# Kernel optimization log

Measured on AMD Instinct MI355X. Metric: run time of the kernel, lower is better.

Reference implementation:

```python
import jax, jax.numpy as jnp
import numpy as np

T, HID, H, KV, D = 2048, 2048, 16, 8, 128
EPS = 1e-6
THETA = 10000.0


def setup_inputs() -> dict:
    key = jax.random.key(0)
    ks = jax.random.split(key, 6)
    positions = jnp.arange(T, dtype=jnp.int64 if jax.config.jax_enable_x64 else jnp.int32)
    hidden_states = jax.random.normal(ks[0], (T, HID), dtype=jnp.float32)
    scale = 0.02
    Wq = jax.random.normal(ks[1], (HID, H * 2 * D), dtype=jnp.float32) * scale
    Wk = jax.random.normal(ks[2], (HID, KV * D), dtype=jnp.float32) * scale
    Wv = jax.random.normal(ks[3], (HID, KV * D), dtype=jnp.float32) * scale
    Wo = jax.random.normal(ks[4], (H * D, HID), dtype=jnp.float32) * scale
    q_norm_w = jnp.zeros((D,), dtype=jnp.float32)  # torch init: zeros, applied as (1+w)
    k_norm_w = jnp.zeros((D,), dtype=jnp.float32)
    return {"positions": positions, "hidden_states": hidden_states, "Wq": Wq,
            "Wk": Wk, "Wv": Wv, "Wo": Wo, "q_norm_w": q_norm_w, "k_norm_w": k_norm_w}


def _rms_norm(x, w):
    # fp32 RMSNorm with (1 + weight) scaling, per last dim
    xf = x.astype(jnp.float32)
    inv = jax.lax.rsqrt(jnp.mean(xf * xf, axis=-1, keepdims=True) + EPS)
    return (xf * inv * (1.0 + w.astype(jnp.float32))).astype(x.dtype)


def _rope(x, positions):
    # neox-style rotary over full head_dim; x: (T, heads, D)
    half = D // 2
    inv_freq = 1.0 / (THETA ** (jnp.arange(0, half, dtype=jnp.float32) / half))
    freqs = positions.astype(jnp.float32)[:, None] * inv_freq  # (T, half)
    cos = jnp.cos(freqs)[:, None, :]  # (T,1,half)
    sin = jnp.sin(freqs)[:, None, :]
    x1, x2 = x[..., :half], x[..., half:]
    return jnp.concatenate([x1 * cos - x2 * sin, x2 * cos + x1 * sin], axis=-1)


def reference(positions, hidden_states, Wq, Wk, Wv, Wo, q_norm_w, k_norm_w):
    scaling = D ** -0.5
    qg = (hidden_states @ Wq).reshape(T, H, 2 * D)
    q, gate = qg[..., :D], qg[..., D:]              # (T,H,D) each
    k = (hidden_states @ Wk).reshape(T, KV, D)
    v = (hidden_states @ Wv).reshape(T, KV, D)
    q = _rms_norm(q, q_norm_w)
    k = _rms_norm(k, k_norm_w)
    q = _rope(q, positions)
    k = _rope(k, positions)
    # GQA: repeat kv heads
    rep = H // KV
    k = jnp.repeat(k, rep, axis=1)                   # (T,H,D)
    v = jnp.repeat(v, rep, axis=1)
    scores = jnp.einsum('thd,shd->hts', q, k) * scaling  # (H,T,T)
    causal = positions[:, None] >= positions[None, :]     # (T,T)
    scores = jnp.where(causal[None], scores, jnp.finfo(scores.dtype).min)
    probs = jax.nn.softmax(scores, axis=-1)
    o = jnp.einsum('hts,shd->thd', probs, v).reshape(T, H * D)
    o = o * jax.nn.sigmoid(gate.reshape(T, H * D))
    return o @ Wo
```

## Files before the change

### kernel.cpp

```cpp
#include <hip/hip_runtime.h>
#include <stdint.h>
#include <math.h>

#define T_SEQ 2048
#define HID   2048
#define NH    16
#define NKV   8
#define DH    128

typedef __bf16 bf16x8 __attribute__((ext_vector_type(8)));
typedef float  f32x4  __attribute__((ext_vector_type(4)));

__device__ __forceinline__ ushort f2bf(float f) {
  uint32_t u = __float_as_uint(f);
  u += 0x7FFF + ((u >> 16) & 1);
  return (ushort)(u >> 16);
}
__device__ __forceinline__ ushort f2bf_rz(float f) {
  return (ushort)(__float_as_uint(f) >> 16);
}
__device__ __forceinline__ float bf2f(ushort u) {
  return __uint_as_float(((uint32_t)u) << 16);
}
__device__ __forceinline__ void gld16(const void* g, void* l) {
  __builtin_amdgcn_global_load_lds(
      (const __attribute__((address_space(1))) uint32_t*)g,
      (__attribute__((address_space(3))) uint32_t*)l, 16, 0, 0);
}

__global__ __launch_bounds__(256) void prep_kernel(
    const float* __restrict__ hs, const float* __restrict__ Wq,
    const float* __restrict__ Wk, const float* __restrict__ Wv,
    const float* __restrict__ Wo, ushort* __restrict__ hs16,
    ushort* __restrict__ Wqt, ushort* __restrict__ Wkt,
    ushort* __restrict__ Wvt, ushort* __restrict__ Wot) {
  int bid = blockIdx.x;
  if (bid < 4096) {
    int i = (bid * 256 + threadIdx.x) * 4;
    float4 v = *(const float4*)(hs + i);
    ushort4 o = {f2bf(v.x), f2bf(v.y), f2bf(v.z), f2bf(v.w)};
    *(ushort4*)(hs16 + i) = o;
    return;
  }
  bid -= 4096;
  const float* src; ushort* dst; int N, bi, bj;
  if (bid < 2048)      { src = Wq; dst = Wqt; N = 4096; bj = bid & 63; bi = bid >> 6; }
  else if (bid < 2560) { bid -= 2048; src = Wk; dst = Wkt; N = 1024; bj = bid & 15; bi = bid >> 4; }
  else if (bid < 3072) { bid -= 2560; src = Wv; dst = Wvt; N = 1024; bj = bid & 15; bi = bid >> 4; }
  else                 { bid -= 3072; src = Wo; dst = Wot; N = 2048; bj = bid & 31; bi = bid >> 5; }
  __shared__ float tile[64][65];
  const int r = threadIdx.x >> 2, cg = (threadIdx.x & 3) * 16;
  const float* sp = src + (size_t)(bi * 64 + r) * N + bj * 64 + cg;
#pragma unroll
  for (int p = 0; p < 4; ++p) {
    float4 v = *(const float4*)(sp + p * 4);
    tile[r][cg + p * 4 + 0] = v.x; tile[r][cg + p * 4 + 1] = v.y;
    tile[r][cg + p * 4 + 2] = v.z; tile[r][cg + p * 4 + 3] = v.w;
  }
  __syncthreads();
  ushort* dp = dst + (size_t)(bj * 64 + r) * HID + bi * 64 + cg;
#pragma unroll
  for (int p = 0; p < 2; ++p) {
    union { uint4 v; ushort u[8]; } o;
#pragma unroll
    for (int j = 0; j < 8; ++j) o.u[j] = f2bf(tile[cg + p * 8 + j][r]);
    *(uint4*)(dp + p * 8) = o.v;
  }
}

template <int MI>
__device__ __forceinline__ void gemm_loop(
    const ushort* __restrict__ A, const ushort* __restrict__ Bt,
    int K, int m0, int n0, ushort* As, ushort* Bs, f32x4 (*acc)[4]) {
  const int tid = threadIdx.x, lane = tid & 63, w = tid >> 6;
  const int quad = lane >> 4, l15 = lane & 15;
  const int wm = (w >> 1) * (MI * 16), wn = (w & 1) * 64;
  const int srow = tid >> 2, sch = tid & 3;
  for (int k0 = 0; k0 < K; k0 += 32) {
    __syncthreads();
#pragma unroll
    for (int p = 0; p < MI / 2; ++p) {
      int row = p * 64 + srow;
      int gch = sch ^ ((row >> 1) & 3);
      gld16(A + (size_t)(m0 + row) * K + k0 + gch * 8,
            As + (p * 256 + w * 64) * 8);
    }
#pragma unroll
    for (int p = 0; p < 2; ++p) {
      int row = p * 64 + srow;
      int gch = sch ^ ((row >> 1) & 3);
      gld16(Bt + (size_t)(n0 + row) * K + k0 + gch * 8,
            Bs + (p * 256 + w * 64) * 8);
    }
    __syncthreads();
    bf16x8 af[MI], bfr[4];
#pragma unroll
    for (int mi = 0; mi < MI; ++mi) {
      int row = wm + mi * 16 + l15;
      int pch = quad ^ ((row >> 1) & 3);
      af[mi] = *(const bf16x8*)(As + row * 32 + pch * 8);
    }
#pragma unroll
    for (int ni = 0; ni < 4; ++ni) {
      int row = wn + ni * 16 + l15;
      int pch = quad ^ ((row >> 1) & 3);
      bfr[ni] = *(const bf16x8*)(Bs + row * 32 + pch * 8);
    }
#pragma unroll
    for (int mi = 0; mi < MI; ++mi)
#pragma unroll
      for (int ni = 0; ni < 4; ++ni)
        acc[mi][ni] = __builtin_amdgcn_mfma_f32_16x16x32_bf16(
            af[mi], bfr[ni], acc[mi][ni], 0, 0, 0);
  }
}

__device__ __forceinline__ void bf16_store(f32x4 (*acc)[4],
                                           ushort* __restrict__ Cb, int Ncols,
                                           int m0, int n0) {
  const int lane = threadIdx.x & 63, w = threadIdx.x >> 6;
  const int quad = lane >> 4, l15 = lane & 15;
  const int wm = (w >> 1) * 64, wn = (w & 1) * 64;
#pragma unroll
  for (int mi = 0; mi < 4; ++mi)
#pragma unroll
    for (int ni = 0; ni < 4; ++ni)
#pragma unroll
      for (int r = 0; r < 4; ++r) {
        int row = m0 + wm + mi * 16 + quad * 4 + r;
        int col = n0 + wn + ni * 16 + l15;
        Cb[(size_t)row * Ncols + col] = f2bf(acc[mi][ni][r]);
      }
}

__global__ __launch_bounds__(256) void gemm_qkv(
    const ushort* __restrict__ hs16, const ushort* __restrict__ Wqt,
    const ushort* __restrict__ Wkt, const ushort* __restrict__ Wvt,
    ushort* __restrict__ qg16, ushort* __restrict__ kb16,
    ushort* __restrict__ v16t) {
  __shared__ ushort As[128 * 32];
  __shared__ ushort Bs[128 * 32];
  f32x4 acc[4][4];
#pragma unroll
  for (int i = 0; i < 4; ++i)
#pragma unroll
    for (int j = 0; j < 4; ++j) acc[i][j] = (f32x4){0.f, 0.f, 0.f, 0.f};
  const int b = blockIdx.x;
  if (b < 512) {
    int m0 = (b >> 5) * 128, n0 = (b & 31) * 128;
    gemm_loop<4>(hs16, Wqt, HID, m0, n0, As, Bs, acc);
    bf16_store(acc, qg16, 4096, m0, n0);
  } else if (b < 640) {
    int f = b - 512, m0 = (f >> 3) * 128, n0 = (f & 7) * 128;
    gemm_loop<4>(hs16, Wkt, HID, m0, n0, As, Bs, acc);
    bf16_store(acc, kb16, 1024, m0, n0);
  } else {
    int f = b - 640, m0 = (f >> 4) * 128, n0 = (f & 15) * 128;
    gemm_loop<4>(Wvt, hs16, HID, m0, n0, As, Bs, acc);
    bf16_store(acc, v16t, T_SEQ, m0, n0);
  }
}

__global__ __launch_bounds__(256) void gemm_out(
    const ushort* __restrict__ ob16, const ushort* __restrict__ Wot,
    float* __restrict__ out) {
  __shared__ ushort As[64 * 32];
  __shared__ ushort Bs[128 * 32];
  f32x4 acc[2][4];
#pragma unroll
  for (int i = 0; i < 2; ++i)
#pragma unroll
    for (int j = 0; j < 4; ++j) acc[i][j] = (f32x4){0.f, 0.f, 0.f, 0.f};
  const int b = blockIdx.x;
  const int m0 = (b >> 4) * 64, n0 = (b & 15) * 128;
  gemm_loop<2>(ob16, Wot, HID, m0, n0, As, Bs, acc);
  const int lane = threadIdx.x & 63, w = threadIdx.x >> 6;
  const int quad = lane >> 4, l15 = lane & 15;
  const int wm = (w >> 1) * 32, wn = (w & 1) * 64;
#pragma unroll
  for (int mi = 0; mi < 2; ++mi)
#pragma unroll
    for (int ni = 0; ni < 4; ++ni)
#pragma unroll
      for (int r = 0; r < 4; ++r) {
        int row = m0 + wm + mi * 16 + quad * 4 + r;
        int col = n0 + wn + ni * 16 + l15;
        out[(size_t)row * HID + col] = acc[mi][ni][r];
      }
}

__global__ __launch_bounds__(128) void norm_k(
    const ushort* __restrict__ kb16, const int* __restrict__ positions,
    const float* __restrict__ kw, ushort* __restrict__ k16) {
  const int t = blockIdx.x, kv = blockIdx.y, d = threadIdx.x;
  const ushort* x = kb16 + ((size_t)t * NKV + kv) * DH;
  ushort* out = k16 + ((size_t)t * NKV + kv) * DH;
  float v = bf2f(x[d]);
  float ss = v * v;
#pragma unroll
  for (int off = 32; off >= 1; off >>= 1) ss += __shfl_xor(ss, off, 64);
  __shared__ float red[2];
  if ((d & 63) == 0) red[d >> 6] = ss;
  __syncthreads();
  float mean = (red[0] + red[1]) * (1.0f / 128.0f);
  float xn = v * rsqrtf(mean + 1e-6f) * (1.0f + kw[d]);
  __shared__ float sh[128];
  sh[d] = xn;
  __syncthreads();
  if (d < 64) {
    float pos = (float)positions[t];
    float rev = pos * exp2f((float)d * -0.20762050593045233f) *
                0.15915494309189535f;
    float fr = rev - floorf(rev);
    float s = __builtin_amdgcn_sinf(fr);
    float c = __builtin_amdgcn_cosf(fr);
    float x1 = sh[d], x2 = sh[d + 64];
    out[d]      = f2bf(x1 * c - x2 * s);
    out[d + 64] = f2bf(x2 * c + x1 * s);
  }
}

__global__ __launch_bounds__(256) void attn_mfma(
    const ushort* __restrict__ qg16, const ushort* __restrict__ k16,
    const ushort* __restrict__ v16t, const int* __restrict__ positions,
    const float* __restrict__ qnw, const float* __restrict__ knw,
    ushort* __restrict__ Op0, ushort* __restrict__ Op1,
    ushort* __restrict__ Op2, float* __restrict__ lpart) {
  const int pb = blockIdx.x, h = blockIdx.y, s = blockIdx.z, kvh = h >> 1;
  const int tid = threadIdx.x, lane = tid & 63, w = tid >> 6;
  const int quad = lane >> 4, l15 = lane & 15;

  __shared__ ushort Ks[64 * 128];
  __shared__ ushort Vs[144 * 64];
  __shared__ ushort Ps[4][16][72];

  for (int i = tid; i < 16 * 64; i += 256) {
    int row = 128 + (i >> 6), col = i & 63;
    Vs[row * 64 + col] = (row == 128) ? (ushort)0x3F80 : (ushort)0;
  }

  __shared__ float s8[8];
  __shared__ float bshare;
  {
    float mq = 0.f, mk = 0.f;
    if (tid < 128) { mq = fabsf(1.f + qnw[tid]); mk = fabsf(1.f + knw[tid]); }
#pragma unroll
    for (int off = 32; off >= 1; off >>= 1) {
      mq = fmaxf(mq, __shfl_xor(mq, off, 64));
      mk = fmaxf(mk, __shfl_xor(mk, off, 64));
    }
    if (lane == 0) { s8[w * 2] = mq; s8[w * 2 + 1] = mk; }
    __syncthreads();
    if (tid == 0) {
      float MQ = fmaxf(s8[0], s8[2]), MK = fmaxf(s8[1], s8[3]);
      bshare = 16.3217f * MQ * MK * 1.02f + 0.1f;
    }
    __syncthreads();
  }
  const float B = bshare;
  const float CSC = 0.08838834764831845f * 1.44269504088896f;

  float wq[4][8];
#pragma unroll
  for (int ks = 0; ks < 4; ++ks)
#pragma unroll
    for (int j = 0; j < 8; ++j) wq[ks][j] = 1.f + qnw[ks * 32 + quad * 8 + j];

#pragma unroll 1
  for (int sel = 0; sel < 2; ++sel) {
    const int qt = sel ? (31 - pb) : pb;
    const int q0 = qt * 64;
    const int ntl = (qt >= s) ? ((qt - s) / 3 + 1) : 0;

    float qv[4][8];
    const ushort* qb = qg16 + ((size_t)(q0 + w * 16 + l15) * NH + h) * (2 * DH);
#pragma unroll
    for (int ks = 0; ks < 4; ++ks) {
      ushort4 u0 = *(const ushort4*)(qb + ks * 32 + quad * 8);
      ushort4 u1 = *(const ushort4*)(qb + ks * 32 + quad * 8 + 4);
      qv[ks][0] = bf2f(u0.x); qv[ks][1] = bf2f(u0.y);
      qv[ks][2] = bf2f(u0.z); qv[ks][3] = bf2f(u0.w);
      qv[ks][4] = bf2f(u1.x); qv[ks][5] = bf2f(u1.y);
      qv[ks][6] = bf2f(u1.z); qv[ks][7] = bf2f(u1.w);
    }
    float ss = 0.f;
#pragma unroll
    for (int ks = 0; ks < 4; ++ks)
#pragma unroll
      for (int j = 0; j < 8; ++j) ss += qv[ks][j] * qv[ks][j];
    ss += __shfl_xor(ss, 16, 64);
    ss += __shfl_xor(ss, 32, 64);
    const float inv = rsqrtf(ss * (1.f / 128.f) + 1e-6f);
    const float pos = (float)positions[q0 + w * 16 + l15];
    union { bf16x8 v; ushort u[8]; } qfu[4];
#pragma unroll
    for (int ks = 0; ks < 2; ++ks)
#pragma unroll
      for (int j = 0; j < 8; ++j) {
        int d = ks * 32 + quad * 8 + j;
        float rev = pos * exp2f((float)d * -0.20762050593045233f) *
                    0.15915494309189535f;
        float fr = rev - floorf(rev);
        float sn = __builtin_amdgcn_sinf(fr);
        float cs = __builtin_amdgcn_cosf(fr);
        float x1 = qv[ks][j] * inv * wq[ks][j];
        float x2 = qv[ks + 2][j] * inv * wq[ks + 2][j];
        qfu[ks].u[j]     = f2bf(x1 * cs - x2 * sn);
        qfu[ks + 2].u[j] = f2bf(x2 * cs + x1 * sn);
      }

    f32x4 oacc[9];
#pragma unroll
    for (int i = 0; i < 9; ++i) oacc[i] = (f32x4){0.f, 0.f, 0.f, 0.f};

#pragma unroll 1
    for (int it = 0; it < ntl; ++it) {
      const int kt = s + 3 * it;
      const int kt0 = kt * 64;
      __syncthreads();
#pragma unroll
      for (int p = 0; p < 4; ++p) {
        int row = p * 16 + (tid >> 4), ch = tid & 15;
        int gch = ch ^ (row & 15);
        gld16(k16 + ((size_t)(kt0 + row) * NKV + kvh) * DH + gch * 8,
              Ks + (p * 256 + w * 64) * 8);
      }
#pragma unroll
      for (int p = 0; p < 4; ++p) {
        int row = p * 32 + (tid >> 3), ch = tid & 7;
        int gch = ch ^ (row & 7);
        gld16(v16t + (size_t)(kvh * DH + row) * T_SEQ + kt0 + gch * 8,
              Vs + (p * 256 + w * 64) * 8);
      }
      __syncthreads();

      f32x4 sacc[4];
#pragma unroll
      for (int ni = 0; ni < 4; ++ni) sacc[ni] = (f32x4){0.f, 0.f, 0.f, 0.f};
#pragma unroll
      for (int ks = 0; ks < 4; ++ks)
#pragma unroll
        for (int ni = 0; ni < 4; ++ni) {
          int row = ni * 16 + l15;
          int pch = (ks * 4 + quad) ^ (row & 15);
          bf16x8 kf = *(const bf16x8*)(Ks + row * 128 + pch * 8);
          sacc[ni] = __builtin_amdgcn_mfma_f32_16x16x32_bf16(
              qfu[ks].v, kf, sacc[ni], 0, 0, 0);
        }

      const bool diag = (kt == qt);
#pragma unroll
      for (int ni = 0; ni < 4; ++ni) {
        int key = kt0 + ni * 16 + l15;
#pragma unroll
        for (int r = 0; r < 4; ++r) {
          float arg = fmaf(sacc[ni][r], CSC, -B);
          float pv;
          if (diag) {
            int q = q0 + w * 16 + quad * 4 + r;
            pv = (key <= q) ? exp2f(arg) : 0.f;
          } else {
            pv = exp2f(arg);
          }
          Ps[w][quad * 4 + r][ni * 16 + l15] = f2bf_rz(pv);
        }
      }

#pragma unroll
      for (int ks2 = 0; ks2 < 2; ++ks2) {
        bf16x8 pf = *(const bf16x8*)(&Ps[w][l15][ks2 * 32 + quad * 8]);
#pragma unroll
        for (int ni = 0; ni < 9; ++ni) {
          int row = ni * 16 + l15;
          int pch = (ks2 * 4 + quad) ^ (row & 7);
          bf16x8 vf = *(const bf16x8*)(Vs + row * 64 + pch * 8);
          oacc[ni] = __builtin_amdgcn_mfma_f32_16x16x32_bf16(
              pf, vf, oacc[ni], 0, 0, 0);
        }
      }
    }

    ushort* Op = (s == 0) ? Op0 : (s == 1) ? Op1 : Op2;
#pragma unroll
    for (int ni = 0; ni < 8; ++ni) {
      int d = ni * 16 + l15;
#pragma unroll
      for (int r = 0; r < 4; ++r) {
        int q = q0 + w * 16 + quad * 4 + r;
        Op[((size_t)h * T_SEQ + q) * DH + d] = f2bf(oacc[ni][r]);
      }
    }
    if (l15 == 0) {
#pragma unroll
      for (int r = 0; r < 4; ++r) {
        int q = q0 + w * 16 + quad * 4 + r;
        lpart[(size_t)s * (NH * T_SEQ) + h * T_SEQ + q] = oacc[8][r];
      }
    }
  }
}

__global__ __launch_bounds__(256) void combine_kernel(
    const ushort* __restrict__ Op0, const ushort* __restrict__ Op1,
    const ushort* __restrict__ Op2, const float* __restrict__ lpart,
    const ushort* __restrict__ qg16, ushort* __restrict__ ob16) {
  const int t = blockIdx.x, tid = threadIdx.x;
  const int h = tid >> 4, d0 = (tid & 15) * 8;
  const int NT = NH * T_SEQ;
  const float l = lpart[h * T_SEQ + t] + lpart[NT + h * T_SEQ + t] +
                  lpart[2 * NT + h * T_SEQ + t];
  const float inv = 1.0f / l;
  const size_t po = ((size_t)h * T_SEQ + t) * DH + d0;
  ushort4 a0 = *(const ushort4*)(Op0 + po);
  ushort4 a1 = *(const ushort4*)(Op0 + po + 4);
  ushort4 b0 = *(const ushort4*)(Op1 + po);
  ushort4 b1 = *(const ushort4*)(Op1 + po + 4);
  ushort4 c0 = *(const ushort4*)(Op2 + po);
  ushort4 c1 = *(const ushort4*)(Op2 + po + 4);
  const ushort* gp = qg16 + ((size_t)t * NH + h) * (2 * DH) + DH + d0;
  ushort4 g0 = *(const ushort4*)(gp);
  ushort4 g1 = *(const ushort4*)(gp + 4);
  float oa[8] = {bf2f(a0.x), bf2f(a0.y), bf2f(a0.z), bf2f(a0.w),
                 bf2f(a1.x), bf2f(a1.y), bf2f(a1.z), bf2f(a1.w)};
  float ob[8] = {bf2f(b0.x), bf2f(b0.y), bf2f(b0.z), bf2f(b0.w),
                 bf2f(b1.x), bf2f(b1.y), bf2f(b1.z), bf2f(b1.w)};
  float oc[8] = {bf2f(c0.x), bf2f(c0.y), bf2f(c0.z), bf2f(c0.w),
                 bf2f(c1.x), bf2f(c1.y), bf2f(c1.z), bf2f(c1.w)};
  float gg[8] = {bf2f(g0.x), bf2f(g0.y), bf2f(g0.z), bf2f(g0.w),
                 bf2f(g1.x), bf2f(g1.y), bf2f(g1.z), bf2f(g1.w)};
  ushort r[8];
#pragma unroll
  for (int i = 0; i < 8; ++i) {
    float o = (oa[i] + ob[i] + oc[i]) * inv;
    o = o / (1.0f + exp2f(-gg[i] * 1.44269504088896f));
    r[i] = f2bf(o);
  }
  ushort* op = ob16 + (size_t)t * (NH * DH) + h * DH + d0;
  *(ushort4*)(op)     = (ushort4){r[0], r[1], r[2], r[3]};
  *(ushort4*)(op + 4) = (ushort4){r[4], r[5], r[6], r[7]};
}

extern "C" void kernel_launch(void* const* d_in, const int* in_sizes, int n_in,
                              void* d_out, int out_size, void* d_ws, size_t ws_size,
                              hipStream_t stream) {
  const int*   positions = (const int*)d_in[0];
  const float* hs  = (const float*)d_in[1];
  const float* Wq  = (const float*)d_in[2];
  const float* Wk  = (const float*)d_in[3];
  const float* Wv  = (const float*)d_in[4];
  const float* Wo  = (const float*)d_in[5];
  const float* qnw = (const float*)d_in[6];
  const float* knw = (const float*)d_in[7];
  float* out = (float*)d_out;

  const size_t MB = 1 << 20;
  uint8_t* ws = (uint8_t*)d_ws;
  ushort* qg16 = (ushort*)(ws + 0);
  ushort* hs16 = (ushort*)(ws + 16 * MB);
  ushort* Op0  = (ushort*)(ws + 16 * MB);
  ushort* Wqt  = (ushort*)(ws + 24 * MB);
  ushort* Op1  = (ushort*)(ws + 24 * MB);
  ushort* Op2  = (ushort*)(ws + 32 * MB);
  ushort* kb16 = (ushort*)(ws + 40 * MB);
  float*  lpart= (float*)(ws + 40 * MB);
  ushort* Wkt  = (ushort*)(ws + 44 * MB);
  ushort* k16  = (ushort*)(ws + 44 * MB);
  ushort* Wvt  = (ushort*)(ws + 48 * MB);
  ushort* ob16 = (ushort*)(ws + 48 * MB);
  ushort* v16t = (ushort*)(ws + 52 * MB);
  ushort* Wot  = (ushort*)(ws + 56 * MB);

  prep_kernel<<<8192, 256, 0, stream>>>(hs, Wq, Wk, Wv, Wo,
                                        hs16, Wqt, Wkt, Wvt, Wot);
  gemm_qkv<<<768, 256, 0, stream>>>(hs16, Wqt, Wkt, Wvt, qg16, kb16, v16t);
  norm_k<<<dim3(T_SEQ, NKV), 128, 0, stream>>>(kb16, positions, knw, k16);
  attn_mfma<<<dim3(16, NH, 3), 256, 0, stream>>>(qg16, k16, v16t, positions,
                                                 qnw, knw, Op0, Op1, Op2, lpart);
  combine_kernel<<<T_SEQ, 256, 0, stream>>>(Op0, Op1, Op2, lpart, qg16, ob16);
  gemm_out<<<512, 256, 0, stream>>>(ob16, Wot, out);
}
```

Measured before the change: 289.5 us.

## Fuse Q/K RMSNorm and RoPE into the QKV GEMM epilogue

Moves the Q and K RMSNorm plus rotary embedding into the QKV GEMM epilogue. It remaps each warp's B-fragment columns so every thread holds both halves of each rotary pair, and reduces the row sum of squares through shared memory. This removes the separate norm_k launch and the per-tile Q norm/RoPE recomputation inside the attention kernel, which now loads pre-rotated bf16 Q directly. Gate is written to its own buffer, the workspace layout is reshuffled, and lpart temporarily lives in the output buffer. The cost is a heavier GEMM epilogue with scattered 2-byte stores and extra syncs.

```diff
diff --git a/kernel.cpp b/kernel.cpp
--- a/kernel.cpp
+++ b/kernel.cpp
@@ -68,13 +68,13 @@
   }
 }
 
-template <int MI>
+template <int MI, int REMAP>
 __device__ __forceinline__ void gemm_loop(
     const ushort* __restrict__ A, const ushort* __restrict__ Bt,
     int K, int m0, int n0, ushort* As, ushort* Bs, f32x4 (*acc)[4]) {
   const int tid = threadIdx.x, lane = tid & 63, w = tid >> 6;
   const int quad = lane >> 4, l15 = lane & 15;
-  const int wm = (w >> 1) * (MI * 16), wn = (w & 1) * 64;
+  const int wm = (w >> 1) * (MI * 16), wn = (w & 1) * 64, p32 = (w & 1) * 32;
   const int srow = tid >> 2, sch = tid & 3;
   for (int k0 = 0; k0 < K; k0 += 32) {
     __syncthreads();
@@ -102,7 +102,8 @@
     }
 #pragma unroll
     for (int ni = 0; ni < 4; ++ni) {
-      int row = wn + ni * 16 + l15;
+      int row = REMAP ? ((ni >> 1) * 64 + p32 + (ni & 1) * 16 + l15)
+                      : (wn + ni * 16 + l15);
       int pch = quad ^ ((row >> 1) & 3);
       bfr[ni] = *(const bf16x8*)(Bs + row * 32 + pch * 8);
     }
@@ -115,28 +116,92 @@
   }
 }
 
-__device__ __forceinline__ void bf16_store(f32x4 (*acc)[4],
-                                           ushort* __restrict__ Cb, int Ncols,
-                                           int m0, int n0) {
+__device__ __forceinline__ int rcol(int ni) {
+  return (ni >> 1) * 64 + ((threadIdx.x >> 6) & 1) * 32 + (ni & 1) * 16 +
+         (threadIdx.x & 15);
+}
+
+__device__ __forceinline__ void bf16_store_r(f32x4 (*acc)[4],
+                                             ushort* __restrict__ Cb,
+                                             int Ncols, int m0, int n0) {
+  const int lane = threadIdx.x & 63, w = threadIdx.x >> 6;
+  const int quad = lane >> 4;
+  const int wm = (w >> 1) * 64;
+#pragma unroll
+  for (int mi = 0; mi < 4; ++mi)
+#pragma unroll
+    for (int ni = 0; ni < 4; ++ni)
+#pragma unroll
+      for (int r = 0; r < 4; ++r) {
+        int row = m0 + wm + mi * 16 + quad * 4 + r;
+        int col = n0 + rcol(ni);
+        Cb[(size_t)row * Ncols + col] = f2bf(acc[mi][ni][r]);
+      }
+}
+
+__device__ __forceinline__ void nr_epilogue(
+    f32x4 (*acc)[4], const float* __restrict__ wgt,
+    const int* __restrict__ positions, int m0, ushort* __restrict__ outp,
+    int ostride, float* psld ) {
   const int lane = threadIdx.x & 63, w = threadIdx.x >> 6;
   const int quad = lane >> 4, l15 = lane & 15;
-  const int wm = (w >> 1) * 64, wn = (w & 1) * 64;
+  const int wm = (w >> 1) * 64, p32 = (w & 1) * 32;
+  float rs[4][4];
 #pragma unroll
   for (int mi = 0; mi < 4; ++mi)
 #pragma unroll
-    for (int ni = 0; ni < 4; ++ni)
-#pragma unroll
-      for (int r = 0; r < 4; ++r) {
-        int row = m0 + wm + mi * 16 + quad * 4 + r;
-        int col = n0 + wn + ni * 16 + l15;
-        Cb[(size_t)row * Ncols + col] = f2bf(acc[mi][ni][r]);
-      }
+    for (int r = 0; r < 4; ++r) {
+      float s = 0.f;
+#pragma unroll
+      for (int ni = 0; ni < 4; ++ni) { float v = acc[mi][ni][r]; s += v * v; }
+#pragma unroll
+      for (int off = 1; off <= 8; off <<= 1) s += __shfl_xor(s, off, 64);
+      rs[mi][r] = s;
+    }
+  __syncthreads();
+  if (l15 == 0) {
+#pragma unroll
+    for (int mi = 0; mi < 4; ++mi)
+#pragma unroll
+      for (int r = 0; r < 4; ++r)
+        psld[(wm + mi * 16 + quad * 4 + r) * 2 + (w & 1)] = rs[mi][r];
+  }
+  __syncthreads();
+  float wv[4];
+#pragma unroll
+  for (int ni = 0; ni < 4; ++ni) wv[ni] = 1.f + wgt[rcol(ni)];
+#pragma unroll
+  for (int mi = 0; mi < 4; ++mi)
+#pragma unroll
+    for (int r = 0; r < 4; ++r) {
+      int row = wm + mi * 16 + quad * 4 + r;
+      int t = m0 + row;
+      float inv = rsqrtf((psld[row * 2] + psld[row * 2 + 1]) * (1.f / 128.f) +
+                         1e-6f);
+      float pos = (float)positions[t];
+      ushort* op = outp + (size_t)t * ostride;
+#pragma unroll
+      for (int ni = 0; ni < 2; ++ni) {
+        int d = p32 + ni * 16 + l15;
+        float rev = pos * exp2f((float)d * -0.20762050593045233f) *
+                    0.15915494309189535f;
+        float fr = rev - floorf(rev);
+        float sn = __builtin_amdgcn_sinf(fr);
+        float cs = __builtin_amdgcn_cosf(fr);
+        float x1 = acc[mi][ni][r] * inv * wv[ni];
+        float x2 = acc[mi][ni + 2][r] * inv * wv[ni + 2];
+        op[d]      = f2bf(x1 * cs - x2 * sn);
+        op[d + 64] = f2bf(x2 * cs + x1 * sn);
+      }
+    }
 }
 
 __global__ __launch_bounds__(256) void gemm_qkv(
     const ushort* __restrict__ hs16, const ushort* __restrict__ Wqt,
     const ushort* __restrict__ Wkt, const ushort* __restrict__ Wvt,
-    ushort* __restrict__ qg16, ushort* __restrict__ kb16,
+    const int* __restrict__ positions, const float* __restrict__ qnw,
+    const float* __restrict__ knw, ushort* __restrict__ q16,
+    ushort* __restrict__ gate16, ushort* __restrict__ k16,
     ushort* __restrict__ v16t) {
   __shared__ ushort As[128 * 32];
   __shared__ ushort Bs[128 * 32];
@@ -147,17 +212,20 @@
     for (int j = 0; j < 4; ++j) acc[i][j] = (f32x4){0.f, 0.f, 0.f, 0.f};
   const int b = blockIdx.x;
   if (b < 512) {
-    int m0 = (b >> 5) * 128, n0 = (b & 31) * 128;
-    gemm_loop<4>(hs16, Wqt, HID, m0, n0, As, Bs, acc);
-    bf16_store(acc, qg16, 4096, m0, n0);
+    int mt = b >> 5, nt = b & 31, m0 = mt * 128, h = nt >> 1;
+    gemm_loop<4, 1>(hs16, Wqt, HID, m0, nt * 128, As, Bs, acc);
+    if ((nt & 1) == 0)
+      nr_epilogue(acc, qnw, positions, m0, q16 + h * DH, NH * DH, (float*)As);
+    else
+      bf16_store_r(acc, gate16, NH * DH, m0, h * DH);
   } else if (b < 640) {
-    int f = b - 512, m0 = (f >> 3) * 128, n0 = (f & 7) * 128;
-    gemm_loop<4>(hs16, Wkt, HID, m0, n0, As, Bs, acc);
-    bf16_store(acc, kb16, 1024, m0, n0);
+    int f = b - 512, mt = f >> 3, nt = f & 7, m0 = mt * 128;
+    gemm_loop<4, 1>(hs16, Wkt, HID, m0, nt * 128, As, Bs, acc);
+    nr_epilogue(acc, knw, positions, m0, k16 + nt * DH, NKV * DH, (float*)As);
   } else {
     int f = b - 640, m0 = (f >> 4) * 128, n0 = (f & 15) * 128;
-    gemm_loop<4>(Wvt, hs16, HID, m0, n0, As, Bs, acc);
-    bf16_store(acc, v16t, T_SEQ, m0, n0);
+    gemm_loop<4, 1>(Wvt, hs16, HID, m0, n0, As, Bs, acc);
+    bf16_store_r(acc, v16t, T_SEQ, m0, n0);
   }
 }
 
@@ -173,7 +241,7 @@
     for (int j = 0; j < 4; ++j) acc[i][j] = (f32x4){0.f, 0.f, 0.f, 0.f};
   const int b = blockIdx.x;
   const int m0 = (b >> 4) * 64, n0 = (b & 15) * 128;
-  gemm_loop<2>(ob16, Wot, HID, m0, n0, As, Bs, acc);
+  gemm_loop<2, 0>(ob16, Wot, HID, m0, n0, As, Bs, acc);
   const int lane = threadIdx.x & 63, w = threadIdx.x >> 6;
   const int quad = lane >> 4, l15 = lane & 15;
   const int wm = (w >> 1) * 32, wn = (w & 1) * 64;
@@ -189,43 +257,12 @@
       }
 }
 
-__global__ __launch_bounds__(128) void norm_k(
-    const ushort* __restrict__ kb16, const int* __restrict__ positions,
-    const float* __restrict__ kw, ushort* __restrict__ k16) {
-  const int t = blockIdx.x, kv = blockIdx.y, d = threadIdx.x;
-  const ushort* x = kb16 + ((size_t)t * NKV + kv) * DH;
-  ushort* out = k16 + ((size_t)t * NKV + kv) * DH;
-  float v = bf2f(x[d]);
-  float ss = v * v;
-#pragma unroll
-  for (int off = 32; off >= 1; off >>= 1) ss += __shfl_xor(ss, off, 64);
-  __shared__ float red[2];
-  if ((d & 63) == 0) red[d >> 6] = ss;
-  __syncthreads();
-  float mean = (red[0] + red[1]) * (1.0f / 128.0f);
-  float xn = v * rsqrtf(mean + 1e-6f) * (1.0f + kw[d]);
-  __shared__ float sh[128];
-  sh[d] = xn;
-  __syncthreads();
-  if (d < 64) {
-    float pos = (float)positions[t];
-    float rev = pos * exp2f((float)d * -0.20762050593045233f) *
-                0.15915494309189535f;
-    float fr = rev - floorf(rev);
-    float s = __builtin_amdgcn_sinf(fr);
-    float c = __builtin_amdgcn_cosf(fr);
-    float x1 = sh[d], x2 = sh[d + 64];
-    out[d]      = f2bf(x1 * c - x2 * s);
-    out[d + 64] = f2bf(x2 * c + x1 * s);
-  }
-}
-
 __global__ __launch_bounds__(256) void attn_mfma(
-    const ushort* __restrict__ qg16, const ushort* __restrict__ k16,
-    const ushort* __restrict__ v16t, const int* __restrict__ positions,
-    const float* __restrict__ qnw, const float* __restrict__ knw,
-    ushort* __restrict__ Op0, ushort* __restrict__ Op1,
-    ushort* __restrict__ Op2, float* __restrict__ lpart) {
+    const ushort* __restrict__ q16, const ushort* __restrict__ k16,
+    const ushort* __restrict__ v16t, const float* __restrict__ qnw,
+    const float* __restrict__ knw, ushort* __restrict__ Op0,
+    ushort* __restrict__ Op1, ushort* __restrict__ Op2,
+    float* __restrict__ lpart) {
   const int pb = blockIdx.x, h = blockIdx.y, s = blockIdx.z, kvh = h >> 1;
   const int tid = threadIdx.x, lane = tid & 63, w = tid >> 6;
   const int quad = lane >> 4, l15 = lane & 15;
@@ -260,54 +297,17 @@
   const float B = bshare;
   const float CSC = 0.08838834764831845f * 1.44269504088896f;
 
-  float wq[4][8];
-#pragma unroll
-  for (int ks = 0; ks < 4; ++ks)
-#pragma unroll
-    for (int j = 0; j < 8; ++j) wq[ks][j] = 1.f + qnw[ks * 32 + quad * 8 + j];
-
 #pragma unroll 1
   for (int sel = 0; sel < 2; ++sel) {
     const int qt = sel ? (31 - pb) : pb;
     const int q0 = qt * 64;
     const int ntl = (qt >= s) ? ((qt - s) / 3 + 1) : 0;
 
-    float qv[4][8];
-    const ushort* qb = qg16 + ((size_t)(q0 + w * 16 + l15) * NH + h) * (2 * DH);
-#pragma unroll
-    for (int ks = 0; ks < 4; ++ks) {
-      ushort4 u0 = *(const ushort4*)(qb + ks * 32 + quad * 8);
-      ushort4 u1 = *(const ushort4*)(qb + ks * 32 + quad * 8 + 4);
-      qv[ks][0] = bf2f(u0.x); qv[ks][1] = bf2f(u0.y);
-      qv[ks][2] = bf2f(u0.z); qv[ks][3] = bf2f(u0.w);
-      qv[ks][4] = bf2f(u1.x); qv[ks][5] = bf2f(u1.y);
-      qv[ks][6] = bf2f(u1.z); qv[ks][7] = bf2f(u1.w);
-    }
-    float ss = 0.f;
+    bf16x8 qf[4];
+    const ushort* qbase = q16 + ((size_t)(q0 + w * 16 + l15) * NH + h) * DH;
 #pragma unroll
     for (int ks = 0; ks < 4; ++ks)
-#pragma unroll
-      for (int j = 0; j < 8; ++j) ss += qv[ks][j] * qv[ks][j];
-    ss += __shfl_xor(ss, 16, 64);
-    ss += __shfl_xor(ss, 32, 64);
-    const float inv = rsqrtf(ss * (1.f / 128.f) + 1e-6f);
-    const float pos = (float)positions[q0 + w * 16 + l15];
-    union { bf16x8 v; ushort u[8]; } qfu[4];
-#pragma unroll
-    for (int ks = 0; ks < 2; ++ks)
-#pragma unroll
-      for (int j = 0; j < 8; ++j) {
-        int d = ks * 32 + quad * 8 + j;
-        float rev = pos * exp2f((float)d * -0.20762050593045233f) *
-                    0.15915494309189535f;
-        float fr = rev - floorf(rev);
-        float sn = __builtin_amdgcn_sinf(fr);
-        float cs = __builtin_amdgcn_cosf(fr);
-        float x1 = qv[ks][j] * inv * wq[ks][j];
-        float x2 = qv[ks + 2][j] * inv * wq[ks + 2][j];
-        qfu[ks].u[j]     = f2bf(x1 * cs - x2 * sn);
-        qfu[ks + 2].u[j] = f2bf(x2 * cs + x1 * sn);
-      }
+      qf[ks] = *(const bf16x8*)(qbase + ks * 32 + quad * 8);
 
     f32x4 oacc[9];
 #pragma unroll
@@ -345,7 +345,7 @@
           int pch = (ks * 4 + quad) ^ (row & 15);
           bf16x8 kf = *(const bf16x8*)(Ks + row * 128 + pch * 8);
           sacc[ni] = __builtin_amdgcn_mfma_f32_16x16x32_bf16(
-              qfu[ks].v, kf, sacc[ni], 0, 0, 0);
+              qf[ks], kf, sacc[ni], 0, 0, 0);
         }
 
       const bool diag = (kt == qt);
@@ -403,7 +403,7 @@
 __global__ __launch_bounds__(256) void combine_kernel(
     const ushort* __restrict__ Op0, const ushort* __restrict__ Op1,
     const ushort* __restrict__ Op2, const float* __restrict__ lpart,
-    const ushort* __restrict__ qg16, ushort* __restrict__ ob16) {
+    const ushort* __restrict__ gate16, ushort* __restrict__ ob16) {
   const int t = blockIdx.x, tid = threadIdx.x;
   const int h = tid >> 4, d0 = (tid & 15) * 8;
   const int NT = NH * T_SEQ;
@@ -417,7 +417,7 @@
   ushort4 b1 = *(const ushort4*)(Op1 + po + 4);
   ushort4 c0 = *(const ushort4*)(Op2 + po);
   ushort4 c1 = *(const ushort4*)(Op2 + po + 4);
-  const ushort* gp = qg16 + ((size_t)t * NH + h) * (2 * DH) + DH + d0;
+  const ushort* gp = gate16 + (size_t)t * (NH * DH) + h * DH + d0;
   ushort4 g0 = *(const ushort4*)(gp);
   ushort4 g1 = *(const ushort4*)(gp + 4);
   float oa[8] = {bf2f(a0.x), bf2f(a0.y), bf2f(a0.z), bf2f(a0.w),
@@ -449,33 +449,34 @@
   const float* Wk  = (const float*)d_in[3];
   const float* Wv  = (const float*)d_in[4];
   const float* Wo  = (const float*)d_in[5];
+  const float* Wo_ = Wo; (void)Wo_;
   const float* qnw = (const float*)d_in[6];
   const float* knw = (const float*)d_in[7];
   float* out = (float*)d_out;
 
   const size_t MB = 1 << 20;
   uint8_t* ws = (uint8_t*)d_ws;
-  ushort* qg16 = (ushort*)(ws + 0);
-  ushort* hs16 = (ushort*)(ws + 16 * MB);
-  ushort* Op0  = (ushort*)(ws + 16 * MB);
-  ushort* Wqt  = (ushort*)(ws + 24 * MB);
-  ushort* Op1  = (ushort*)(ws + 24 * MB);
-  ushort* Op2  = (ushort*)(ws + 32 * MB);
-  ushort* kb16 = (ushort*)(ws + 40 * MB);
-  float*  lpart= (float*)(ws + 40 * MB);
-  ushort* Wkt  = (ushort*)(ws + 44 * MB);
-  ushort* k16  = (ushort*)(ws + 44 * MB);
-  ushort* Wvt  = (ushort*)(ws + 48 * MB);
-  ushort* ob16 = (ushort*)(ws + 48 * MB);
-  ushort* v16t = (ushort*)(ws + 52 * MB);
-  ushort* Wot  = (ushort*)(ws + 56 * MB);
+  ushort* hs16  = (ushort*)(ws + 0);
+  ushort* Op0   = (ushort*)(ws + 0);
+  ushort* Wqt   = (ushort*)(ws + 8 * MB);
+  ushort* Op1   = (ushort*)(ws + 8 * MB);
+  ushort* Op2   = (ushort*)(ws + 16 * MB);
+  ushort* Wkt   = (ushort*)(ws + 24 * MB);
+  ushort* ob16  = (ushort*)(ws + 24 * MB);
+  ushort* Wvt   = (ushort*)(ws + 28 * MB);
+  ushort* v16t  = (ushort*)(ws + 32 * MB);
+  ushort* k16   = (ushort*)(ws + 36 * MB);
+  ushort* q16   = (ushort*)(ws + 40 * MB);
+  ushort* gate16= (ushort*)(ws + 48 * MB);
+  ushort* Wot   = (ushort*)(ws + 56 * MB);
+  float*  lpart = (float*)d_out;
 
   prep_kernel<<<8192, 256, 0, stream>>>(hs, Wq, Wk, Wv, Wo,
                                         hs16, Wqt, Wkt, Wvt, Wot);
-  gemm_qkv<<<768, 256, 0, stream>>>(hs16, Wqt, Wkt, Wvt, qg16, kb16, v16t);
-  norm_k<<<dim3(T_SEQ, NKV), 128, 0, stream>>>(kb16, positions, knw, k16);
-  attn_mfma<<<dim3(16, NH, 3), 256, 0, stream>>>(qg16, k16, v16t, positions,
-                                                 qnw, knw, Op0, Op1, Op2, lpart);
-  combine_kernel<<<T_SEQ, 256, 0, stream>>>(Op0, Op1, Op2, lpart, qg16, ob16);
+  gemm_qkv<<<768, 256, 0, stream>>>(hs16, Wqt, Wkt, Wvt, positions, qnw, knw,
+                                    q16, gate16, k16, v16t);
+  attn_mfma<<<dim3(16, NH, 3), 256, 0, stream>>>(q16, k16, v16t, qnw, knw,
+                                                 Op0, Op1, Op2, lpart);
+  combine_kernel<<<T_SEQ, 256, 0, stream>>>(Op0, Op1, Op2, lpart, gate16, ob16);
   gemm_out<<<512, 256, 0, stream>>>(ob16, Wot, out);
 }
```

After: 286.4 us. About the same (-1.1%).
